# Kernel optimization log

Hardware: AMD Instinct MI355X
Metric: run time of the kernel (lower is better)

Reference implementation:

```python
import jax, jax.numpy as jnp
import numpy as np

B, L, D, H, DH, FF = 4, 1024, 1024, 16, 64, 4096
EPS = 1e-5


def _layer_norm(x, g, b):
    m = jnp.mean(x, -1, keepdims=True)
    v = jnp.mean((x - m) ** 2, -1, keepdims=True)
    return (x - m) * jax.lax.rsqrt(v + EPS) * g + b


def setup_inputs() -> dict:
    key = jax.random.key(0)
    ks = jax.random.split(key, 20)
    s = 0.02  # param init scale
    return {
        "x": jax.random.normal(ks[0], (B, L, D), jnp.float32),
        "adj_mask_matrix": jax.random.uniform(ks[1], (B * H, L, L), jnp.float32),
        "com_mask_matrix": jax.random.uniform(ks[2], (B * H, L, L), jnp.float32),
        "lattice_rel": jax.random.normal(ks[3], (2, 1, 1, DH), jnp.float32),
        "Wq": jax.random.normal(ks[4], (D, D), jnp.float32) * s,
        "bq": jnp.zeros((D,), jnp.float32),
        "Wk": jax.random.normal(ks[5], (D, D), jnp.float32) * s,
        "bk": jnp.zeros((D,), jnp.float32),
        "Wv": jax.random.normal(ks[6], (D, D), jnp.float32) * s,
        "bv": jnp.zeros((D,), jnp.float32),
        "Wo": jax.random.normal(ks[7], (D, D), jnp.float32) * s,
        "bo": jnp.zeros((D,), jnp.float32),
        "ln1_scale": jnp.ones((D,), jnp.float32),
        "ln1_bias": jnp.zeros((D,), jnp.float32),
        "W1": jax.random.normal(ks[8], (D, FF), jnp.float32) * s,
        "b1": jnp.zeros((FF,), jnp.float32),
        "W2": jax.random.normal(ks[9], (FF, D), jnp.float32) * s,
        "b2": jnp.zeros((D,), jnp.float32),
        "ln2_scale": jnp.ones((D,), jnp.float32),
        "ln2_bias": jnp.zeros((D,), jnp.float32),
    }


def reference(x, adj_mask_matrix, com_mask_matrix, lattice_rel,
              Wq, bq, Wk, bk, Wv, bv, Wo, bo, ln1_scale, ln1_bias,
              W1, b1, W2, b2, ln2_scale, ln2_bias):
    Bsz, Ln, Dm = x.shape
    # QKV projections; flat reshape [B,L,H*dh] -> [B*H,L,dh] matches torch .view
    Q = (x @ Wq + bq).reshape(Bsz * H, Ln, DH)
    K = (x @ Wk + bk).reshape(Bsz * H, Ln, DH)
    V = (x @ Wv + bv).reshape(Bsz * H, Ln, DH)
    scale = DH ** (-0.5)
    adj_rel = lattice_rel[0]  # [1,1,dh] broadcasts over (B*H, L)
    com_rel = lattice_rel[1]
    att_adj = jnp.einsum('bqd,bkd->bqk', Q + adj_rel, K + adj_rel) * scale
    att_com = jnp.einsum('bqd,bkd->bqk', Q + com_rel, K + com_rel) * scale
    # post-softmax multiplicative masking, then sum of the two attention maps
    mask_att = (jax.nn.softmax(att_adj, axis=-1) * adj_mask_matrix
                + jax.nn.softmax(att_com, axis=-1) * com_mask_matrix)
    context = jnp.matmul(mask_att, V).reshape(Bsz, Ln, H * DH)
    out = _layer_norm(context @ Wo + bo + x, ln1_scale, ln1_bias)
    ff = jax.nn.relu(out @ W1 + b1) @ W2 + b2
    return _layer_norm(ff + out, ln2_scale, ln2_bias)
```

## Files before the change

### kernel.cpp

```cpp
#include <hip/hip_runtime.h>
#include <hip/hip_bf16.h>

typedef __attribute__((ext_vector_type(8))) short s16x8;
typedef __attribute__((ext_vector_type(4))) float f32x4;
typedef unsigned short u16;
typedef unsigned int u32;

__device__ __forceinline__ u16 f2b(float f) {
    u32 u = __float_as_uint(f);
    u32 r = (u + 0x7fffu + ((u >> 16) & 1u)) >> 16;
    return (u16)r;
}
__device__ __forceinline__ float b2f(u16 b) {
    return __uint_as_float(((u32)b) << 16);
}

#define MFMA16(a, b, c) __builtin_amdgcn_mfma_f32_16x16x32_bf16(a, b, c, 0, 0, 0)
#define GLDS(gp, lp)                                                              \
    __builtin_amdgcn_global_load_lds((const __attribute__((address_space(1))) void*)(gp), \
                                     (__attribute__((address_space(3))) void*)(lp), 16, 0, 0)

__global__ void k_f2b(const float* __restrict__ in, u16* __restrict__ out, int n4) {
    int i = blockIdx.x * 256 + threadIdx.x;
    if (i >= n4) return;
    float4 v = ((const float4*)in)[i];
    ushort4 o;
    o.x = f2b(v.x); o.y = f2b(v.y); o.z = f2b(v.z); o.w = f2b(v.w);
    ((ushort4*)out)[i] = o;
}

__global__ void k_wtrans(const float* __restrict__ W, u16* __restrict__ Wt, int K, int N) {
    __shared__ float t[32][33];
    int bx = blockIdx.x * 32, by = blockIdx.y * 32;
    int tx = threadIdx.x, ty = threadIdx.y;
    for (int i = 0; i < 32; i += 8)
        t[ty + i][tx] = W[(size_t)(by + ty + i) * N + bx + tx];
    __syncthreads();
    for (int i = 0; i < 32; i += 8)
        Wt[(size_t)(bx + ty + i) * K + by + tx] = f2b(t[tx][ty + i]);
}

__global__ __launch_bounds__(256) void gemm_qkv(const u16* __restrict__ A, const u16* __restrict__ Bt,
                                                const float* __restrict__ bq, const float* __restrict__ bk,
                                                const float* __restrict__ bv,
                                                u16* __restrict__ Qb, u16* __restrict__ Kb,
                                                u16* __restrict__ Vt) {
    __shared__ __align__(16) short lA[128 * 64];
    __shared__ __align__(16) short lB[128 * 64];
    const int tid = threadIdx.x, lane = tid & 63, w = tid >> 6;
    const int l15 = lane & 15, lg = lane >> 4;
    const int wr = w >> 1, wc = w & 1;
    const int m0 = blockIdx.y * 128, n0 = blockIdx.x * 128;
    const int KK = 1024;
    f32x4 acc[4][4] = {};

    for (int k0 = 0; k0 < KK; k0 += 64) {
        #pragma unroll
        for (int i = 0; i < 4; i++) {
            int chunk = w * 4 + i;
            int arow = m0 + chunk * 8 + (lane >> 3);
            GLDS(A + (size_t)arow * KK + k0 + (lane & 7) * 8, (short*)lA + chunk * 512);
            int brow = n0 + chunk * 8 + (lane >> 3);
            GLDS(Bt + (size_t)brow * KK + k0 + (lane & 7) * 8, (short*)lB + chunk * 512);
        }
        __syncthreads();
        #pragma unroll
        for (int ks = 0; ks < 2; ks++) {
            s16x8 af[4], bfr[4];
            #pragma unroll
            for (int m = 0; m < 4; m++)
                af[m] = *(const s16x8*)&lA[(wr * 64 + m * 16 + l15) * 64 + ks * 32 + lg * 8];
            #pragma unroll
            for (int n = 0; n < 4; n++)
                bfr[n] = *(const s16x8*)&lB[(wc * 64 + n * 16 + l15) * 64 + ks * 32 + lg * 8];
            #pragma unroll
            for (int m = 0; m < 4; m++)
                #pragma unroll
                for (int n = 0; n < 4; n++)
                    acc[m][n] = MFMA16(af[m], bfr[n], acc[m][n]);
        }
        __syncthreads();
    }
    const int rbase = m0 + wr * 64, cbase = n0 + wc * 64;
    const int seg = cbase >> 10;
    #pragma unroll
    for (int m = 0; m < 4; m++)
        #pragma unroll
        for (int n = 0; n < 4; n++) {
            int col = cbase + n * 16 + l15;
            int c1 = col & 1023, d = col & 63;
            int row0 = rbase + m * 16 + lg * 4;
            if (seg == 0) {
                float bb = bq[c1];
                #pragma unroll
                for (int r = 0; r < 4; r++)
                    Qb[(size_t)(row0 + r) * 1024 + c1] = f2b(acc[m][n][r] + bb);
            } else if (seg == 1) {
                float bb = bk[c1];
                #pragma unroll
                for (int r = 0; r < 4; r++)
                    Kb[(size_t)(row0 + r) * 1024 + c1] = f2b(acc[m][n][r] + bb);
            } else {
                float bb = bv[c1];
                #pragma unroll
                for (int r = 0; r < 4; r++) {
                    int row = row0 + r;
                    size_t o = (size_t)(row >> 6) * 65536 + (size_t)d * 1024 + (row & 63) * 16 + (c1 >> 6);
                    Vt[o] = f2b(acc[m][n][r] + bb);
                }
            }
        }
}

template <int EPI>
__global__ __launch_bounds__(256) void gemm_bt(const u16* __restrict__ A, const u16* __restrict__ Bt,
                                               void* __restrict__ Cv, int M, int N, int K,
                                               const float* __restrict__ bias) {
    __shared__ __align__(16) short lA[128 * 64];
    __shared__ __align__(16) short lB[128 * 64];
    const int tid = threadIdx.x, lane = tid & 63, w = tid >> 6;
    const int l15 = lane & 15, lg = lane >> 4;
    const int wr = w >> 1, wc = w & 1;
    const int m0 = blockIdx.y * 128, n0 = blockIdx.x * 128;
    f32x4 acc[4][4] = {};

    for (int k0 = 0; k0 < K; k0 += 64) {
        #pragma unroll
        for (int i = 0; i < 4; i++) {
            int chunk = w * 4 + i;
            int arow = m0 + chunk * 8 + (lane >> 3);
            GLDS(A + (size_t)arow * K + k0 + (lane & 7) * 8, (short*)lA + chunk * 512);
            int brow = n0 + chunk * 8 + (lane >> 3);
            GLDS(Bt + (size_t)brow * K + k0 + (lane & 7) * 8, (short*)lB + chunk * 512);
        }
        __syncthreads();
        #pragma unroll
        for (int ks = 0; ks < 2; ks++) {
            s16x8 af[4], bfr[4];
            #pragma unroll
            for (int m = 0; m < 4; m++)
                af[m] = *(const s16x8*)&lA[(wr * 64 + m * 16 + l15) * 64 + ks * 32 + lg * 8];
            #pragma unroll
            for (int n = 0; n < 4; n++)
                bfr[n] = *(const s16x8*)&lB[(wc * 64 + n * 16 + l15) * 64 + ks * 32 + lg * 8];
            #pragma unroll
            for (int m = 0; m < 4; m++)
                #pragma unroll
                for (int n = 0; n < 4; n++)
                    acc[m][n] = MFMA16(af[m], bfr[n], acc[m][n]);
        }
        __syncthreads();
    }
    const int rbase = m0 + wr * 64, cbase = n0 + wc * 64;
    #pragma unroll
    for (int m = 0; m < 4; m++)
        #pragma unroll
        for (int n = 0; n < 4; n++) {
            int col = cbase + n * 16 + l15;
            int row0 = rbase + m * 16 + lg * 4;
            u16* C = (u16*)Cv;
            float bv = bias[col];
            #pragma unroll
            for (int r = 0; r < 4; r++)
                C[(size_t)(row0 + r) * N + col] = f2b(fmaxf(acc[m][n][r] + bv, 0.f));
        }
}

__global__ __launch_bounds__(256) void gemm_bt64(const u16* __restrict__ A, const u16* __restrict__ Bt,
                                                 float* __restrict__ C, int M, int N, int K) {
    __shared__ __align__(16) short lA[128 * 64];
    __shared__ __align__(16) short lB[64 * 64];
    const int tid = threadIdx.x, lane = tid & 63, w = tid >> 6;
    const int l15 = lane & 15, lg = lane >> 4;
    const int m0 = blockIdx.y * 128, n0 = blockIdx.x * 64;
    f32x4 acc[2][4] = {};

    for (int k0 = 0; k0 < K; k0 += 64) {
        #pragma unroll
        for (int i = 0; i < 4; i++) {
            int chunk = w * 4 + i;
            int arow = m0 + chunk * 8 + (lane >> 3);
            GLDS(A + (size_t)arow * K + k0 + (lane & 7) * 8, (short*)lA + chunk * 512);
        }
        #pragma unroll
        for (int i = 0; i < 2; i++) {
            int chunk = w * 2 + i;
            int brow = n0 + chunk * 8 + (lane >> 3);
            GLDS(Bt + (size_t)brow * K + k0 + (lane & 7) * 8, (short*)lB + chunk * 512);
        }
        __syncthreads();
        #pragma unroll
        for (int ks = 0; ks < 2; ks++) {
            s16x8 af[2], bfr[4];
            #pragma unroll
            for (int m = 0; m < 2; m++)
                af[m] = *(const s16x8*)&lA[(w * 32 + m * 16 + l15) * 64 + ks * 32 + lg * 8];
            #pragma unroll
            for (int n = 0; n < 4; n++)
                bfr[n] = *(const s16x8*)&lB[(n * 16 + l15) * 64 + ks * 32 + lg * 8];
            #pragma unroll
            for (int m = 0; m < 2; m++)
                #pragma unroll
                for (int n = 0; n < 4; n++)
                    acc[m][n] = MFMA16(af[m], bfr[n], acc[m][n]);
        }
        __syncthreads();
    }
    #pragma unroll
    for (int m = 0; m < 2; m++)
        #pragma unroll
        for (int n = 0; n < 4; n++) {
            int col = n0 + n * 16 + l15;
            int row0 = m0 + w * 32 + m * 16 + lg * 4;
            #pragma unroll
            for (int r = 0; r < 4; r++)
                C[(size_t)(row0 + r) * N + col] = acc[m][n][r];
        }
}

__global__ void k_fvec(const u16* __restrict__ Kb, const float* __restrict__ rel,
                       float* __restrict__ fa, float* __restrict__ fc) {
    __shared__ float rs[128];
    const int g = blockIdx.x, tid = threadIdx.x;
    if (tid < 128) rs[tid] = rel[tid];
    __syncthreads();
    for (int k = tid; k < 1024; k += 256) {
        const u16* kr = Kb + (size_t)g * 65536 + (size_t)k * 64;
        float sa = 0.f, sc = 0.f;
        #pragma unroll
        for (int j = 0; j < 8; j++) {
            s16x8 v = *(const s16x8*)(kr + j * 8);
            #pragma unroll
            for (int e = 0; e < 8; e++) {
                float kv = b2f((u16)v[e]);
                sa += kv * rs[j * 8 + e];
                sc += kv * rs[64 + j * 8 + e];
            }
        }
        fa[g * 1024 + k] = __expf(sa * 0.125f);
        fc[g * 1024 + k] = __expf(sc * 0.125f);
    }
}

__global__ __launch_bounds__(256, 2) void k_qke0(const u16* __restrict__ Qb, const u16* __restrict__ Kb,
                                                 const float* __restrict__ fa, const float* __restrict__ fc,
                                                 u16* __restrict__ E0,
                                                 float* __restrict__ la_, float* __restrict__ lc_) {
    const int bid = blockIdx.x;
    const int xcd = bid & 7, j = bid >> 3;
    const int g = xcd * 8 + (j & 7), qt = j >> 3;
    const int tid = threadIdx.x, lane = tid & 63, w = tid >> 6;
    const int l15 = lane & 15, lg = lane >> 4;
    __shared__ __align__(16) float lE[4][16][68];

    const int q0 = qt * 64 + w * 16;
    const size_t gQ = (size_t)g * 65536;
    const float scale = 0.125f;

    s16x8 qf[2];
    #pragma unroll
    for (int ks = 0; ks < 2; ks++)
        qf[ks] = *(const s16x8*)(Qb + gQ + (size_t)(q0 + l15) * 64 + ks * 32 + lg * 8);

    float la[4] = {0.f, 0.f, 0.f, 0.f}, lc[4] = {0.f, 0.f, 0.f, 0.f};
    const int srow = lane >> 2, sjj = lane & 3;

    #pragma unroll 1
    for (int it = 0; it < 16; it++) {
        const int kb = it * 64;
        f32x4 sa[4] = {};
        s16x8 kf[8];
        #pragma unroll
        for (int ks = 0; ks < 2; ks++)
            #pragma unroll
            for (int n = 0; n < 4; n++)
                kf[ks * 4 + n] = *(const s16x8*)(Kb + gQ + (size_t)(kb + n * 16 + l15) * 64 + ks * 32 + lg * 8);
        #pragma unroll
        for (int ks = 0; ks < 2; ks++)
            #pragma unroll
            for (int n = 0; n < 4; n++)
                sa[n] = MFMA16(qf[ks], kf[ks * 4 + n], sa[n]);
        #pragma unroll
        for (int n = 0; n < 4; n++) {
            float fav = fa[g * 1024 + kb + n * 16 + l15];
            float fcv = fc[g * 1024 + kb + n * 16 + l15];
            #pragma unroll
            for (int r = 0; r < 4; r++) {
                float er = b2f(f2b(__expf(sa[n][r] * scale)));
                la[r] += er * fav;
                lc[r] += er * fcv;
                lE[w][lg * 4 + r][n * 16 + l15] = er;
            }
        }
        {
            const float* lp = &lE[w][srow][sjj * 16];
            uint4 p0, p1;
            p0.x = (u32)f2b(lp[0]) | ((u32)f2b(lp[1]) << 16);
            p0.y = (u32)f2b(lp[2]) | ((u32)f2b(lp[3]) << 16);
            p0.z = (u32)f2b(lp[4]) | ((u32)f2b(lp[5]) << 16);
            p0.w = (u32)f2b(lp[6]) | ((u32)f2b(lp[7]) << 16);
            p1.x = (u32)f2b(lp[8]) | ((u32)f2b(lp[9]) << 16);
            p1.y = (u32)f2b(lp[10]) | ((u32)f2b(lp[11]) << 16);
            p1.z = (u32)f2b(lp[12]) | ((u32)f2b(lp[13]) << 16);
            p1.w = (u32)f2b(lp[14]) | ((u32)f2b(lp[15]) << 16);
            u16* ep = E0 + (size_t)g * 1048576 + (size_t)(q0 + srow) * 1024 + kb + sjj * 16;
            *(uint4*)ep = p0;
            *(uint4*)(ep + 8) = p1;
        }
    }
    #pragma unroll
    for (int r = 0; r < 4; r++)
        #pragma unroll
        for (int m = 8; m >= 1; m >>= 1) {
            la[r] += __shfl_xor(la[r], m);
            lc[r] += __shfl_xor(lc[r], m);
        }
    if (l15 == 0) {
        #pragma unroll
        for (int r = 0; r < 4; r++) {
            la_[g * 1024 + q0 + lg * 4 + r] = la[r];
            lc_[g * 1024 + q0 + lg * 4 + r] = lc[r];
        }
    }
}

__global__ __launch_bounds__(256) void gemm_pvf(const u16* __restrict__ E0, const u16* __restrict__ Vt,
                                                const float* __restrict__ Ma_g, const float* __restrict__ Mc_g,
                                                const float* __restrict__ fa, const float* __restrict__ fc,
                                                const float* __restrict__ la, const float* __restrict__ lc,
                                                u16* __restrict__ ctx) {
    __shared__ __align__(16) float bufMa[64 * 64];
    __shared__ __align__(16) float bufMc[64 * 64];
    __shared__ __align__(16) short bufP[64 * 68];
    __shared__ __align__(16) short bufV[64 * 68];
    __shared__ __align__(16) float lfa[1024];
    __shared__ __align__(16) float lfc[1024];

    const int bid = blockIdx.x;
    const int xcd = bid & 7, j = bid >> 3;
    const int g = xcd * 8 + (j & 7), qt = j >> 3;
    const int tid = threadIdx.x, lane = tid & 63, w = tid >> 6;
    const int l15 = lane & 15, lg = lane >> 4;
    const int q0 = qt * 64;
    const size_t gE = (size_t)g * 1048576;
    const size_t gV = (size_t)g * 65536;

    GLDS(fa + g * 1024 + w * 256 + (lane & 63) * 4, lfa + w * 256);
    GLDS(fc + g * 1024 + w * 256 + (lane & 63) * 4, lfc + w * 256);
    const int pr = tid >> 2, pc = (tid & 3) * 16;
    const float ila = 1.f / la[g * 1024 + q0 + pr];
    const float ilc = 1.f / lc[g * 1024 + q0 + pr];
    const int vd = tid >> 2, vc = (tid & 3) * 16;

    f32x4 acc[4] = {};
    __syncthreads();

    #pragma unroll 1
    for (int it = 0; it < 16; it++) {
        const int kb = it * 64;
        #pragma unroll
        for (int o = 0; o < 4; o++) {
            int op = w * 4 + o;
            int row = op * 4 + (lane >> 4);
            int ch = lane & 15;
            GLDS(Ma_g + (size_t)g * 1048576 + (size_t)(q0 + row) * 1024 + kb + ch * 4, bufMa + op * 256);
            GLDS(Mc_g + (size_t)g * 1048576 + (size_t)(q0 + row) * 1024 + kb + ch * 4, bufMc + op * 256);
        }
        s16x8 v0 = *(const s16x8*)(Vt + gV + (size_t)vd * 1024 + kb + vc);
        s16x8 v1 = *(const s16x8*)(Vt + gV + (size_t)vd * 1024 + kb + vc + 8);
        s16x8 e0 = *(const s16x8*)(E0 + gE + (size_t)(q0 + pr) * 1024 + kb + pc);
        s16x8 e1 = *(const s16x8*)(E0 + gE + (size_t)(q0 + pr) * 1024 + kb + pc + 8);
        *(s16x8*)&bufV[vd * 68 + vc] = v0;
        *(s16x8*)&bufV[vd * 68 + vc + 8] = v1;
        __syncthreads();
        {
            const float* map = &bufMa[pr * 64 + pc];
            const float* mcp = &bufMc[pr * 64 + pc];
            const float* fap = &lfa[kb + pc];
            const float* fcp = &lfc[kb + pc];
            union { s16x8 v; u16 u[8]; } o0, o1;
            #pragma unroll
            for (int e = 0; e < 8; e++) {
                float t = fap[e] * map[e] * ila + fcp[e] * mcp[e] * ilc;
                o0.u[e] = f2b(b2f((u16)e0[e]) * t);
            }
            #pragma unroll
            for (int e = 0; e < 8; e++) {
                float t = fap[8 + e] * map[8 + e] * ila + fcp[8 + e] * mcp[8 + e] * ilc;
                o1.u[e] = f2b(b2f((u16)e1[e]) * t);
            }
            *(s16x8*)&bufP[pr * 68 + pc] = o0.v;
            *(s16x8*)&bufP[pr * 68 + pc + 8] = o1.v;
        }
        __syncthreads();
        #pragma unroll
        for (int ks = 0; ks < 2; ks++) {
            s16x8 af = *(const s16x8*)&bufP[(w * 16 + l15) * 68 + ks * 32 + lg * 8];
            #pragma unroll
            for (int n = 0; n < 4; n++) {
                s16x8 bfr = *(const s16x8*)&bufV[(n * 16 + l15) * 68 + ks * 32 + lg * 8];
                acc[n] = MFMA16(af, bfr, acc[n]);
            }
        }
        __syncthreads();
    }
    #pragma unroll
    for (int n = 0; n < 4; n++) {
        int col = n * 16 + l15;
        int row0 = q0 + w * 16 + lg * 4;
        #pragma unroll
        for (int r = 0; r < 4; r++)
            ctx[gV + (size_t)(row0 + r) * 64 + col] = f2b(acc[n][r]);
    }
}

__global__ __launch_bounds__(256) void k_ln(const float* __restrict__ a, const float* __restrict__ bias,
                                            const float* __restrict__ resid, const float* __restrict__ gamma,
                                            const float* __restrict__ beta, float* __restrict__ out,
                                            u16* __restrict__ outb) {
    const int row = blockIdx.x, tid = threadIdx.x;
    const size_t base = (size_t)row * 1024 + tid * 4;
    float4 av = *(const float4*)(a + base);
    float4 rv = *(const float4*)(resid + base);
    float4 bv = *(const float4*)(bias + tid * 4);
    float t0 = av.x + rv.x + bv.x, t1 = av.y + rv.y + bv.y;
    float t2 = av.z + rv.z + bv.z, t3 = av.w + rv.w + bv.w;
    __shared__ float red[4];
    float s = t0 + t1 + t2 + t3;
    #pragma unroll
    for (int m = 32; m >= 1; m >>= 1) s += __shfl_xor(s, m);
    int w = tid >> 6;
    if ((tid & 63) == 0) red[w] = s;
    __syncthreads();
    float mean = (red[0] + red[1] + red[2] + red[3]) * (1.f / 1024.f);
    float d0 = t0 - mean, d1 = t1 - mean, d2 = t2 - mean, d3 = t3 - mean;
    float q = d0 * d0 + d1 * d1 + d2 * d2 + d3 * d3;
    __syncthreads();
    #pragma unroll
    for (int m = 32; m >= 1; m >>= 1) q += __shfl_xor(q, m);
    if ((tid & 63) == 0) red[w] = q;
    __syncthreads();
    float var = (red[0] + red[1] + red[2] + red[3]) * (1.f / 1024.f);
    float rs = rsqrtf(var + 1e-5f);
    float4 gv = *(const float4*)(gamma + tid * 4);
    float4 bev = *(const float4*)(beta + tid * 4);
    float o0 = d0 * rs * gv.x + bev.x, o1 = d1 * rs * gv.y + bev.y;
    float o2 = d2 * rs * gv.z + bev.z, o3 = d3 * rs * gv.w + bev.w;
    *(float4*)(out + base) = make_float4(o0, o1, o2, o3);
    if (outb) {
        ushort4 ob;
        ob.x = f2b(o0); ob.y = f2b(o1); ob.z = f2b(o2); ob.w = f2b(o3);
        *(ushort4*)(outb + base) = ob;
    }
}

extern "C" void kernel_launch(void* const* d_in, const int* in_sizes, int n_in,
                              void* d_out, int out_size, void* d_ws, size_t ws_size,
                              hipStream_t stream) {
    const float* x    = (const float*)d_in[0];
    const float* adjm = (const float*)d_in[1];
    const float* comm = (const float*)d_in[2];
    const float* rel  = (const float*)d_in[3];
    const float* Wq   = (const float*)d_in[4];
    const float* bq   = (const float*)d_in[5];
    const float* Wk   = (const float*)d_in[6];
    const float* bk   = (const float*)d_in[7];
    const float* Wv   = (const float*)d_in[8];
    const float* bv   = (const float*)d_in[9];
    const float* Wo   = (const float*)d_in[10];
    const float* bo   = (const float*)d_in[11];
    const float* g1   = (const float*)d_in[12];
    const float* be1  = (const float*)d_in[13];
    const float* W1   = (const float*)d_in[14];
    const float* b1   = (const float*)d_in[15];
    const float* W2   = (const float*)d_in[16];
    const float* b2   = (const float*)d_in[17];
    const float* g2   = (const float*)d_in[18];
    const float* be2  = (const float*)d_in[19];
    float* out = (float*)d_out;

    char* ws = (char*)d_ws;
    const size_t MB = 1048576;
    u16*   xb    = (u16*)(ws + 0 * MB);
    u16*   Wqkvt = (u16*)(ws + 8 * MB);
    u16*   Wot   = (u16*)(ws + 14 * MB);
    u16*   W1t   = (u16*)(ws + 16 * MB);
    u16*   W2t   = (u16*)(ws + 24 * MB);
    u16*   Qb    = (u16*)(ws + 32 * MB);
    u16*   Kb    = (u16*)(ws + 40 * MB);
    u16*   Vtb   = (u16*)(ws + 48 * MB);
    float* faB   = (float*)(ws + 56 * MB);
    float* fcB   = (float*)(ws + 56 * MB + 262144);
    float* laB   = (float*)(ws + 56 * MB + 524288);
    float* lcB   = (float*)(ws + 56 * MB + 786432);
    u16*   E0b   = (u16*)(ws + 57 * MB);
    u16*   ctx   = (u16*)(ws + 185 * MB);
    float* ctxWo = (float*)(ws + 193 * MB);
    float* out1  = (float*)(ws + 209 * MB);
    u16*   out1b = (u16*)(ws + 225 * MB);
    u16*   rb    = (u16*)(ws + 233 * MB);
    float* ff2   = (float*)(ws + 265 * MB);

    dim3 tb(32, 8);
    k_f2b<<<4096, 256, 0, stream>>>(x, xb, 1048576);
    k_wtrans<<<dim3(32, 32), tb, 0, stream>>>(Wq, Wqkvt, 1024, 1024);
    k_wtrans<<<dim3(32, 32), tb, 0, stream>>>(Wk, Wqkvt + 1024 * 1024, 1024, 1024);
    k_wtrans<<<dim3(32, 32), tb, 0, stream>>>(Wv, Wqkvt + 2 * 1024 * 1024, 1024, 1024);
    k_wtrans<<<dim3(32, 32), tb, 0, stream>>>(Wo, Wot, 1024, 1024);
    k_wtrans<<<dim3(128, 32), tb, 0, stream>>>(W1, W1t, 1024, 4096);
    k_wtrans<<<dim3(32, 128), tb, 0, stream>>>(W2, W2t, 4096, 1024);
    gemm_qkv<<<dim3(24, 32), 256, 0, stream>>>(xb, Wqkvt, bq, bk, bv, Qb, Kb, Vtb);
    k_fvec<<<64, 256, 0, stream>>>(Kb, rel, faB, fcB);
    k_qke0<<<1024, 256, 0, stream>>>(Qb, Kb, faB, fcB, E0b, laB, lcB);
    gemm_pvf<<<1024, 256, 0, stream>>>(E0b, Vtb, adjm, comm, faB, fcB, laB, lcB, ctx);
    gemm_bt64<<<dim3(16, 32), 256, 0, stream>>>(ctx, Wot, ctxWo, 4096, 1024, 1024);
    k_ln<<<4096, 256, 0, stream>>>(ctxWo, bo, x, g1, be1, out1, out1b);
    gemm_bt<1><<<dim3(32, 32), 256, 0, stream>>>(out1b, W1t, rb, 4096, 4096, 1024, b1);
    gemm_bt64<<<dim3(16, 32), 256, 0, stream>>>(rb, W2t, ff2, 4096, 1024, 4096);
    k_ln<<<4096, 256, 0, stream>>>(ff2, b2, out1, g2, be2, out, nullptr);
}
```

Baseline: 548.2 us.

## Software-pipeline mask, V and E loads in the masked PV GEMM kernel

Restructures the gemm_pvf main loop so that the next tile's mask tiles (Ma/Mc) and V tile are issued as asynchronous global-to-LDS copies while the current tile's MFMAs run. The E0 values and fa/fc scale factors for the next tile are prefetched into registers instead of being read from LDS each iteration. This aims to hide global memory latency in a kernel that streams two large float mask matrices. In exchange it raises register pressure. The V tile now sits in LDS with an unpadded 64-element row stride and the P tile's padding is shrunk, which may add LDS bank conflicts on the fragment reads.

```diff
diff --git a/kernel.cpp b/kernel.cpp
--- a/kernel.cpp
+++ b/kernel.cpp
@@ -329,12 +329,10 @@
                                                 const float* __restrict__ fa, const float* __restrict__ fc,
                                                 const float* __restrict__ la, const float* __restrict__ lc,
                                                 u16* __restrict__ ctx) {
-    __shared__ __align__(16) float bufMa[64 * 64];
-    __shared__ __align__(16) float bufMc[64 * 64];
-    __shared__ __align__(16) short bufP[64 * 68];
-    __shared__ __align__(16) short bufV[64 * 68];
-    __shared__ __align__(16) float lfa[1024];
-    __shared__ __align__(16) float lfc[1024];
+    __shared__ __align__(16) float bufMa[4096];
+    __shared__ __align__(16) float bufMc[4096];
+    __shared__ __align__(16) short bufV[4096];
+    __shared__ __align__(16) short bufP[64 * 66];
 
     const int bid = blockIdx.x;
     const int xcd = bid & 7, j = bid >> 3;
@@ -344,66 +342,98 @@
     const int q0 = qt * 64;
     const size_t gE = (size_t)g * 1048576;
     const size_t gV = (size_t)g * 65536;
-
-    GLDS(fa + g * 1024 + w * 256 + (lane & 63) * 4, lfa + w * 256);
-    GLDS(fc + g * 1024 + w * 256 + (lane & 63) * 4, lfc + w * 256);
+    const size_t gM = (size_t)g * 1048576;
+
     const int pr = tid >> 2, pc = (tid & 3) * 16;
     const float ila = 1.f / la[g * 1024 + q0 + pr];
     const float ilc = 1.f / lc[g * 1024 + q0 + pr];
-    const int vd = tid >> 2, vc = (tid & 3) * 16;
+
+#define STAGE_M(IT)                                                                              \
+    do {                                                                                         \
+        const int kb_ = (IT) * 64;                                                               \
+        _Pragma("unroll") for (int o = 0; o < 4; o++) {                                          \
+            int op = w * 4 + o;                                                                  \
+            int mr = op * 4 + (lane >> 4);                                                       \
+            GLDS(Ma_g + gM + (size_t)(q0 + mr) * 1024 + kb_ + (lane & 15) * 4, bufMa + op * 256);\
+            GLDS(Mc_g + gM + (size_t)(q0 + mr) * 1024 + kb_ + (lane & 15) * 4, bufMc + op * 256);\
+        }                                                                                        \
+    } while (0)
+#define STAGE_V(IT)                                                                              \
+    do {                                                                                         \
+        const int kb_ = (IT) * 64;                                                               \
+        _Pragma("unroll") for (int o = 0; o < 2; o++) {                                          \
+            int op = w * 2 + o;                                                                  \
+            int vr = op * 8 + (lane >> 3);                                                       \
+            GLDS(Vt + gV + (size_t)vr * 1024 + kb_ + (lane & 7) * 8, bufV + op * 512);           \
+        }                                                                                        \
+    } while (0)
+#define LOAD_EF(IT, EA, EB, FAR, FCR)                                                            \
+    do {                                                                                         \
+        const int kb_ = (IT) * 64;                                                               \
+        EA = *(const s16x8*)(E0 + gE + (size_t)(q0 + pr) * 1024 + kb_ + pc);                     \
+        EB = *(const s16x8*)(E0 + gE + (size_t)(q0 + pr) * 1024 + kb_ + pc + 8);                 \
+        _Pragma("unroll") for (int q_ = 0; q_ < 4; q_++) {                                       \
+            FAR[q_] = *(const float4*)(fa + g * 1024 + kb_ + pc + q_ * 4);                       \
+            FCR[q_] = *(const float4*)(fc + g * 1024 + kb_ + pc + q_ * 4);                       \
+        }                                                                                        \
+    } while (0)
 
     f32x4 acc[4] = {};
+    s16x8 eA, eB, eA_n, eB_n;
+    float4 faR[4], fcR[4], faN[4], fcN[4];
+
+    STAGE_M(0);
+    STAGE_V(0);
+    LOAD_EF(0, eA, eB, faR, fcR);
     __syncthreads();
 
     #pragma unroll 1
     for (int it = 0; it < 16; it++) {
-        const int kb = it * 64;
-        #pragma unroll
-        for (int o = 0; o < 4; o++) {
-            int op = w * 4 + o;
-            int row = op * 4 + (lane >> 4);
-            int ch = lane & 15;
-            GLDS(Ma_g + (size_t)g * 1048576 + (size_t)(q0 + row) * 1024 + kb + ch * 4, bufMa + op * 256);
-            GLDS(Mc_g + (size_t)g * 1048576 + (size_t)(q0 + row) * 1024 + kb + ch * 4, bufMc + op * 256);
-        }
-        s16x8 v0 = *(const s16x8*)(Vt + gV + (size_t)vd * 1024 + kb + vc);
-        s16x8 v1 = *(const s16x8*)(Vt + gV + (size_t)vd * 1024 + kb + vc + 8);
-        s16x8 e0 = *(const s16x8*)(E0 + gE + (size_t)(q0 + pr) * 1024 + kb + pc);
-        s16x8 e1 = *(const s16x8*)(E0 + gE + (size_t)(q0 + pr) * 1024 + kb + pc + 8);
-        *(s16x8*)&bufV[vd * 68 + vc] = v0;
-        *(s16x8*)&bufV[vd * 68 + vc + 8] = v1;
-        __syncthreads();
         {
             const float* map = &bufMa[pr * 64 + pc];
             const float* mcp = &bufMc[pr * 64 + pc];
-            const float* fap = &lfa[kb + pc];
-            const float* fcp = &lfc[kb + pc];
+            const float* fap = (const float*)faR;
+            const float* fcp = (const float*)fcR;
             union { s16x8 v; u16 u[8]; } o0, o1;
             #pragma unroll
             for (int e = 0; e < 8; e++) {
                 float t = fap[e] * map[e] * ila + fcp[e] * mcp[e] * ilc;
-                o0.u[e] = f2b(b2f((u16)e0[e]) * t);
+                o0.u[e] = f2b(b2f((u16)eA[e]) * t);
             }
             #pragma unroll
             for (int e = 0; e < 8; e++) {
                 float t = fap[8 + e] * map[8 + e] * ila + fcp[8 + e] * mcp[8 + e] * ilc;
-                o1.u[e] = f2b(b2f((u16)e1[e]) * t);
+                o1.u[e] = f2b(b2f((u16)eB[e]) * t);
             }
-            *(s16x8*)&bufP[pr * 68 + pc] = o0.v;
-            *(s16x8*)&bufP[pr * 68 + pc + 8] = o1.v;
-        }
-        __syncthreads();
+            *(s16x8*)&bufP[pr * 66 + pc] = o0.v;
+            *(s16x8*)&bufP[pr * 66 + pc + 8] = o1.v;
+        }
+        __syncthreads();
+        if (it < 15) {
+            STAGE_M(it + 1);
+            LOAD_EF(it + 1, eA_n, eB_n, faN, fcN);
+        }
         #pragma unroll
         for (int ks = 0; ks < 2; ks++) {
-            s16x8 af = *(const s16x8*)&bufP[(w * 16 + l15) * 68 + ks * 32 + lg * 8];
+            s16x8 af = *(const s16x8*)&bufP[(w * 16 + l15) * 66 + ks * 32 + lg * 8];
             #pragma unroll
             for (int n = 0; n < 4; n++) {
-                s16x8 bfr = *(const s16x8*)&bufV[(n * 16 + l15) * 68 + ks * 32 + lg * 8];
+                s16x8 bfr = *(const s16x8*)&bufV[(n * 16 + l15) * 64 + ks * 32 + lg * 8];
                 acc[n] = MFMA16(af, bfr, acc[n]);
             }
         }
         __syncthreads();
-    }
+        if (it < 15) {
+            STAGE_V(it + 1);
+            eA = eA_n; eB = eB_n;
+            #pragma unroll
+            for (int q_ = 0; q_ < 4; q_++) { faR[q_] = faN[q_]; fcR[q_] = fcN[q_]; }
+        }
+    }
+#undef STAGE_M
+#undef STAGE_V
+#undef LOAD_EF
+
     #pragma unroll
     for (int n = 0; n < 4; n++) {
         int col = n * 16 + l15;
```

After: 553.0 us (median of 2 runs). About the same (+0.9%).

## Replace LDS-staged PV kernel with direct register loads into MFMA fragments

Applied to the files above, without the earlier changes.

The masked P·V kernel no longer stages mask tiles, E0, V and the scaled P tile through shared memory with three barriers per iteration. Each lane now loads its mask rows, E0 and f-vectors straight from global memory in MFMA fragment layout, builds the bf16 P fragment in registers, and reads V fragments directly from global. This removes LDS traffic and synchronisation from a memory-bound kernel. In exchange the global access pattern becomes less coalesced (16 rows per wave, 32-byte chunks) and V is re-read from L2 by every wave.

```diff
diff --git a/kernel.cpp b/kernel.cpp
--- a/kernel.cpp
+++ b/kernel.cpp
@@ -324,85 +324,61 @@
     }
 }
 
-__global__ __launch_bounds__(256) void gemm_pvf(const u16* __restrict__ E0, const u16* __restrict__ Vt,
-                                                const float* __restrict__ Ma_g, const float* __restrict__ Mc_g,
-                                                const float* __restrict__ fa, const float* __restrict__ fc,
-                                                const float* __restrict__ la, const float* __restrict__ lc,
-                                                u16* __restrict__ ctx) {
-    __shared__ __align__(16) float bufMa[64 * 64];
-    __shared__ __align__(16) float bufMc[64 * 64];
-    __shared__ __align__(16) short bufP[64 * 68];
-    __shared__ __align__(16) short bufV[64 * 68];
-    __shared__ __align__(16) float lfa[1024];
-    __shared__ __align__(16) float lfc[1024];
-
+__global__ __launch_bounds__(256) void k_pv3(const u16* __restrict__ E0, const u16* __restrict__ Vt,
+                                             const float* __restrict__ Ma_g, const float* __restrict__ Mc_g,
+                                             const float* __restrict__ fa, const float* __restrict__ fc,
+                                             const float* __restrict__ la, const float* __restrict__ lc,
+                                             u16* __restrict__ ctx) {
     const int bid = blockIdx.x;
     const int xcd = bid & 7, j = bid >> 3;
     const int g = xcd * 8 + (j & 7), qt = j >> 3;
     const int tid = threadIdx.x, lane = tid & 63, w = tid >> 6;
     const int l15 = lane & 15, lg = lane >> 4;
     const int q0 = qt * 64;
+    const int row = q0 + w * 16 + l15;
     const size_t gE = (size_t)g * 1048576;
     const size_t gV = (size_t)g * 65536;
 
-    GLDS(fa + g * 1024 + w * 256 + (lane & 63) * 4, lfa + w * 256);
-    GLDS(fc + g * 1024 + w * 256 + (lane & 63) * 4, lfc + w * 256);
-    const int pr = tid >> 2, pc = (tid & 3) * 16;
-    const float ila = 1.f / la[g * 1024 + q0 + pr];
-    const float ilc = 1.f / lc[g * 1024 + q0 + pr];
-    const int vd = tid >> 2, vc = (tid & 3) * 16;
-
-    f32x4 acc[4] = {};
-    __syncthreads();
+    const float* __restrict__ mrowA = Ma_g + gE + (size_t)row * 1024;
+    const float* __restrict__ mrowC = Mc_g + gE + (size_t)row * 1024;
+    const u16* __restrict__ erow = E0 + gE + (size_t)row * 1024;
+    const float* __restrict__ fag = fa + g * 1024;
+    const float* __restrict__ fcg = fc + g * 1024;
+    const float ila = 1.f / la[g * 1024 + row];
+    const float ilc = 1.f / lc[g * 1024 + row];
+
+    f32x4 ca[4] = {};
 
     #pragma unroll 1
     for (int it = 0; it < 16; it++) {
         const int kb = it * 64;
         #pragma unroll
-        for (int o = 0; o < 4; o++) {
-            int op = w * 4 + o;
-            int row = op * 4 + (lane >> 4);
-            int ch = lane & 15;
-            GLDS(Ma_g + (size_t)g * 1048576 + (size_t)(q0 + row) * 1024 + kb + ch * 4, bufMa + op * 256);
-            GLDS(Mc_g + (size_t)g * 1048576 + (size_t)(q0 + row) * 1024 + kb + ch * 4, bufMc + op * 256);
-        }
-        s16x8 v0 = *(const s16x8*)(Vt + gV + (size_t)vd * 1024 + kb + vc);
-        s16x8 v1 = *(const s16x8*)(Vt + gV + (size_t)vd * 1024 + kb + vc + 8);
-        s16x8 e0 = *(const s16x8*)(E0 + gE + (size_t)(q0 + pr) * 1024 + kb + pc);
-        s16x8 e1 = *(const s16x8*)(E0 + gE + (size_t)(q0 + pr) * 1024 + kb + pc + 8);
-        *(s16x8*)&bufV[vd * 68 + vc] = v0;
-        *(s16x8*)&bufV[vd * 68 + vc + 8] = v1;
-        __syncthreads();
-        {
-            const float* map = &bufMa[pr * 64 + pc];
-            const float* mcp = &bufMc[pr * 64 + pc];
-            const float* fap = &lfa[kb + pc];
-            const float* fcp = &lfc[kb + pc];
-            union { s16x8 v; u16 u[8]; } o0, o1;
-            #pragma unroll
-            for (int e = 0; e < 8; e++) {
-                float t = fap[e] * map[e] * ila + fcp[e] * mcp[e] * ilc;
-                o0.u[e] = f2b(b2f((u16)e0[e]) * t);
+        for (int ks = 0; ks < 2; ks++) {
+            const int kc = kb + ks * 32 + lg * 8;
+            float4 m0 = *(const float4*)(mrowA + kc);
+            float4 m1 = *(const float4*)(mrowA + kc + 4);
+            float4 n0 = *(const float4*)(mrowC + kc);
+            float4 n1 = *(const float4*)(mrowC + kc + 4);
+            s16x8 e = *(const s16x8*)(erow + kc);
+            float4 a0 = *(const float4*)(fag + kc);
+            float4 a1 = *(const float4*)(fag + kc + 4);
+            float4 c0 = *(const float4*)(fcg + kc);
+            float4 c1 = *(const float4*)(fcg + kc + 4);
+            union { s16x8 v; u16 u[8]; } pf;
+            pf.u[0] = f2b(b2f((u16)e[0]) * (a0.x * m0.x * ila + c0.x * n0.x * ilc));
+            pf.u[1] = f2b(b2f((u16)e[1]) * (a0.y * m0.y * ila + c0.y * n0.y * ilc));
+            pf.u[2] = f2b(b2f((u16)e[2]) * (a0.z * m0.z * ila + c0.z * n0.z * ilc));
+            pf.u[3] = f2b(b2f((u16)e[3]) * (a0.w * m0.w * ila + c0.w * n0.w * ilc));
+            pf.u[4] = f2b(b2f((u16)e[4]) * (a1.x * m1.x * ila + c1.x * n1.x * ilc));
+            pf.u[5] = f2b(b2f((u16)e[5]) * (a1.y * m1.y * ila + c1.y * n1.y * ilc));
+            pf.u[6] = f2b(b2f((u16)e[6]) * (a1.z * m1.z * ila + c1.z * n1.z * ilc));
+            pf.u[7] = f2b(b2f((u16)e[7]) * (a1.w * m1.w * ila + c1.w * n1.w * ilc));
+            #pragma unroll
+            for (int d = 0; d < 4; d++) {
+                s16x8 vf = *(const s16x8*)(Vt + gV + (size_t)(d * 16 + l15) * 1024 + kc);
+                ca[d] = MFMA16(pf.v, vf, ca[d]);
             }
-            #pragma unroll
-            for (int e = 0; e < 8; e++) {
-                float t = fap[8 + e] * map[8 + e] * ila + fcp[8 + e] * mcp[8 + e] * ilc;
-                o1.u[e] = f2b(b2f((u16)e1[e]) * t);
-            }
-            *(s16x8*)&bufP[pr * 68 + pc] = o0.v;
-            *(s16x8*)&bufP[pr * 68 + pc + 8] = o1.v;
-        }
-        __syncthreads();
-        #pragma unroll
-        for (int ks = 0; ks < 2; ks++) {
-            s16x8 af = *(const s16x8*)&bufP[(w * 16 + l15) * 68 + ks * 32 + lg * 8];
-            #pragma unroll
-            for (int n = 0; n < 4; n++) {
-                s16x8 bfr = *(const s16x8*)&bufV[(n * 16 + l15) * 68 + ks * 32 + lg * 8];
-                acc[n] = MFMA16(af, bfr, acc[n]);
-            }
-        }
-        __syncthreads();
+        }
     }
     #pragma unroll
     for (int n = 0; n < 4; n++) {
@@ -410,7 +386,7 @@
         int row0 = q0 + w * 16 + lg * 4;
         #pragma unroll
         for (int r = 0; r < 4; r++)
-            ctx[gV + (size_t)(row0 + r) * 64 + col] = f2b(acc[n][r]);
+            ctx[gV + (size_t)(row0 + r) * 64 + col] = f2b(ca[n][r]);
     }
 }
 
@@ -512,7 +488,7 @@
     gemm_qkv<<<dim3(24, 32), 256, 0, stream>>>(xb, Wqkvt, bq, bk, bv, Qb, Kb, Vtb);
     k_fvec<<<64, 256, 0, stream>>>(Kb, rel, faB, fcB);
     k_qke0<<<1024, 256, 0, stream>>>(Qb, Kb, faB, fcB, E0b, laB, lcB);
-    gemm_pvf<<<1024, 256, 0, stream>>>(E0b, Vtb, adjm, comm, faB, fcB, laB, lcB, ctx);
+    k_pv3<<<1024, 256, 0, stream>>>(E0b, Vtb, adjm, comm, faB, fcB, laB, lcB, ctx);
     gemm_bt64<<<dim3(16, 32), 256, 0, stream>>>(ctx, Wot, ctxWo, 4096, 1024, 1024);
     k_ln<<<4096, 256, 0, stream>>>(ctxWo, bo, x, g1, be1, out1, out1b);
     gemm_bt<1><<<dim3(32, 32), 256, 0, stream>>>(out1b, W1t, rb, 4096, 4096, 1024, b1);
```

Result: slower. 575.2 us (+4.9%).
